# Kernel tuning notes

Measured on AMD Instinct MI355X. Metric: run time of the kernel, lower is better.

Reference implementation:

```python
import jax, jax.numpy as jnp
import numpy as np

ALPHA = 0.5    # SpikeAct surrogate width (act_fun(alpha=0.5))
DECAY = 0.2    # membrane decay
THRESH = 0.5   # firing threshold (requires_grad=False -> constant)


@jax.custom_vjp
def spike_act(x):
    # Heaviside spike with rectangular surrogate gradient
    return (x > 0).astype(x.dtype)

def _sa_fwd(x):
    return spike_act(x), x

def _sa_bwd(x, g):
    return (g * (jnp.abs(x) < ALPHA).astype(g.dtype),)

spike_act.defvjp(_sa_fwd, _sa_bwd)


@jax.custom_vjp
def ei_act(x):
    # EI sign gate with straight-through gradient
    return jnp.sign(x)

def _ei_fwd(x):
    return ei_act(x), None

def _ei_bwd(_, g):
    return (g,)

ei_act.defvjp(_ei_fwd, _ei_bwd)


def conv2d(x, w, b):
    # x: [B,C,H,W], w: [O,I,kh,kw] (OIHW), SAME padding, stride 1
    y = jax.lax.conv_general_dilated(
        x, w, window_strides=(1, 1), padding='SAME',
        dimension_numbers=('NCHW', 'OIHW', 'NCHW'))
    return y + b[None, :, None, None]


def setup_inputs() -> dict:
    key = jax.random.key(0)
    k0, k1, k2 = jax.random.split(key, 3)
    T, B, C, H, W, K = 8, 16, 128, 32, 32, 5
    fan_in = C * K * K
    x = jax.random.normal(k0, (T, B, C, H, W), jnp.float32)
    back_w = jax.random.normal(k1, (C, C, K, K), jnp.float32) / np.float32(np.sqrt(fan_in))
    back_b = jnp.zeros((C,), jnp.float32)
    ei_w = jax.random.normal(k2, (C, C, K, K), jnp.float32) / np.float32(np.sqrt(fan_in))
    ei_b = jnp.zeros((C,), jnp.float32)
    return {"x": x, "back_w": back_w, "back_b": back_b, "ei_w": ei_w, "ei_b": ei_b}


def reference(x, back_w, back_b, ei_w, ei_b):
    # x: [T,B,C,H,W] -> spikes over time [T,B,C,H,W]
    state_shape = x.shape[1:]
    mem0 = jnp.zeros(state_shape, x.dtype)
    spike0 = jnp.zeros(state_shape, x.dtype)

    def step(carry, xt):
        mem, spike = carry
        # integral: decayed mem + feedback-conv sigmoid gate * input
        mem = DECAY * mem + jax.nn.sigmoid(conv2d(spike, back_w, back_b)) * xt
        # calc_spike (if_ei=True path)
        ei_gate = ei_act(conv2d(mem, ei_w, ei_b))
        s = spike_act(mem - THRESH)
        mem = mem * (1.0 - s)
        spike = ei_gate * s
        return (mem, spike), spike

    _, spikes = jax.lax.scan(step, (mem0, spike0), x)
    return spikes
```

## Files before the change

kernel.cpp:

```cpp
#include <hip/hip_runtime.h>
#include <math.h>

#define TDIM 512
#define CCH  128
#define HW   32
#define OCT  4
#define ICT  4
#define NPH  16
#define SW   36
#define SROWS 36
#define PLANE (SROWS * SW)

template<int EPI>
__global__ __launch_bounds__(TDIM, 2) void lif_conv(
    const float* __restrict__ cin,
    const float* __restrict__ wgt,
    const float* __restrict__ bias,
    const float* __restrict__ aux0,
    const float* __restrict__ aux1,
    float* __restrict__ out0,
    float* __restrict__ out1,
    int first)
{
    const int ocg  = blockIdx.x;
    const int b    = blockIdx.y;
    const int oc0  = ocg * OCT;
    const int tid  = threadIdx.x;
    const int team = tid >> 8;
    const int lt   = tid & 255;
    const int rl   = lt >> 3;
    const int cl   = (lt & 7) * 4;

    const int steam = __builtin_amdgcn_readfirstlane(team);

    __shared__ __align__(16) float s_in[2 * ICT * PLANE];
    float* tin = s_in + team * (ICT * PLANE);

    float acc[OCT][4];
#pragma unroll
    for (int oc = 0; oc < OCT; ++oc)
#pragma unroll
        for (int j = 0; j < 4; ++j) acc[oc][j] = 0.f;

    if (!(EPI == 0 && first)) {
        const int icbase  = team * 64;
        const int sicbase = steam * 64;
        for (int i = lt; i < ICT * PLANE; i += 256) tin[i] = 0.f;
        __syncthreads();

        const int sr = lt >> 3;
        const int sg = lt & 7;

        for (int ph = 0; ph < NPH; ++ph) {
#pragma unroll
            for (int p = 0; p < ICT; ++p) {
                float4 v = *(const float4*)&cin[(((size_t)b * CCH + icbase + ph * ICT + p) * HW + sr) * HW + sg * 4];
                float* dst = &tin[p * PLANE + (sr + 2) * SW + 2 + sg * 4];
                *(float2*)dst       = make_float2(v.x, v.y);
                *(float2*)(dst + 2) = make_float2(v.z, v.w);
            }
            __syncthreads();
#pragma unroll
            for (int ici = 0; ici < ICT; ++ici) {
                float win5[5][8];
#pragma unroll
                for (int kh = 0; kh < 5; ++kh) {
                    const float* src = &tin[ici * PLANE + (rl + kh) * SW + cl];
                    float4 a = *(const float4*)src;
                    float4 c = *(const float4*)(src + 4);
                    win5[kh][0] = a.x; win5[kh][1] = a.y; win5[kh][2] = a.z; win5[kh][3] = a.w;
                    win5[kh][4] = c.x; win5[kh][5] = c.y; win5[kh][6] = c.z; win5[kh][7] = c.w;
                }
                const float* wb = wgt + ((size_t)oc0 * CCH + sicbase + ph * ICT + ici) * 25;
#pragma unroll
                for (int oc = 0; oc < OCT; ++oc) {
                    const float* wo = wb + oc * (CCH * 25);
#pragma unroll
                    for (int kh = 0; kh < 5; ++kh) {
#pragma unroll
                        for (int kw = 0; kw < 5; ++kw) {
                            float wv = wo[kh * 5 + kw];
                            acc[oc][0] += win5[kh][kw]     * wv;
                            acc[oc][1] += win5[kh][kw + 1] * wv;
                            acc[oc][2] += win5[kh][kw + 2] * wv;
                            acc[oc][3] += win5[kh][kw + 3] * wv;
                        }
                    }
                }
            }
            __syncthreads();
        }

        float* sred = s_in;
        if (team == 1) {
#pragma unroll
            for (int oc = 0; oc < OCT; ++oc)
#pragma unroll
                for (int j = 0; j < 4; ++j)
                    sred[lt * 17 + oc * 4 + j] = acc[oc][j];
        }
        __syncthreads();
        if (team == 0) {
#pragma unroll
            for (int oc = 0; oc < OCT; ++oc)
#pragma unroll
                for (int j = 0; j < 4; ++j)
                    acc[oc][j] += sred[lt * 17 + oc * 4 + j];
        }
    }

    if (team == 0) {
#pragma unroll
        for (int oc = 0; oc < OCT; ++oc) {
            const size_t pidx = (((size_t)b * CCH + oc0 + oc) * HW + rl) * HW + cl;
            const float bia = bias[oc0 + oc];
            float y[4];
#pragma unroll
            for (int j = 0; j < 4; ++j) y[j] = acc[oc][j] + bia;
            if (EPI == 0) {
                float4 xv = *(const float4*)(aux1 + pidx);
                float4 mv;
                if (first) { mv.x = mv.y = mv.z = mv.w = 0.f; }
                else       mv = *(const float4*)(aux0 + pidx);
                float4 mp;
                mp.x = 0.2f * mv.x + (1.f / (1.f + expf(-y[0]))) * xv.x;
                mp.y = 0.2f * mv.y + (1.f / (1.f + expf(-y[1]))) * xv.y;
                mp.z = 0.2f * mv.z + (1.f / (1.f + expf(-y[2]))) * xv.z;
                mp.w = 0.2f * mv.w + (1.f / (1.f + expf(-y[3]))) * xv.w;
                *(float4*)(out0 + pidx) = mp;
            } else {
                float4 m4 = *(const float4*)(aux0 + pidx);
                float g[4] = {
                    (y[0] > 0.f) ? 1.f : ((y[0] < 0.f) ? -1.f : 0.f),
                    (y[1] > 0.f) ? 1.f : ((y[1] < 0.f) ? -1.f : 0.f),
                    (y[2] > 0.f) ? 1.f : ((y[2] < 0.f) ? -1.f : 0.f),
                    (y[3] > 0.f) ? 1.f : ((y[3] < 0.f) ? -1.f : 0.f)};
                float m[4] = {m4.x, m4.y, m4.z, m4.w};
                float4 mn, sp;
                float s0 = (m[0] > 0.5f) ? 1.f : 0.f;
                float s1 = (m[1] > 0.5f) ? 1.f : 0.f;
                float s2 = (m[2] > 0.5f) ? 1.f : 0.f;
                float s3 = (m[3] > 0.5f) ? 1.f : 0.f;
                mn.x = m[0] * (1.f - s0); sp.x = g[0] * s0;
                mn.y = m[1] * (1.f - s1); sp.y = g[1] * s1;
                mn.z = m[2] * (1.f - s2); sp.z = g[2] * s2;
                mn.w = m[3] * (1.f - s3); sp.w = g[3] * s3;
                *(float4*)(out0 + pidx) = mn;
                *(float4*)(out1 + pidx) = sp;
            }
        }
    }
}

extern "C" void kernel_launch(void* const* d_in, const int* in_sizes, int n_in,
                              void* d_out, int out_size, void* d_ws, size_t ws_size,
                              hipStream_t stream) {
    const float* x      = (const float*)d_in[0];
    const float* back_w = (const float*)d_in[1];
    const float* back_b = (const float*)d_in[2];
    const float* ei_w   = (const float*)d_in[3];
    const float* ei_b   = (const float*)d_in[4];
    float* out = (float*)d_out;

    const size_t N = (size_t)16 * CCH * HW * HW;
    float* mem_cur  = (float*)d_ws;
    float* mem_post = mem_cur + N;

    dim3 grid(CCH / OCT, 16);

    for (int t = 0; t < 8; ++t) {
        const float* spike_prev = (t == 0) ? x : (out + (size_t)(t - 1) * N);
        lif_conv<0><<<grid, TDIM, 0, stream>>>(
            spike_prev, back_w, back_b,
            mem_cur, x + (size_t)t * N,
            mem_post, nullptr, (t == 0) ? 1 : 0);
        lif_conv<1><<<grid, TDIM, 0, stream>>>(
            mem_post, ei_w, ei_b,
            mem_post, nullptr,
            mem_cur, out + (size_t)t * N, 0);
    }
}
```

Baseline: 2.128 ms.

## Split each image into row halves and use four input-channel teams per block

```diff
diff --git a/kernel.cpp b/kernel.cpp
--- a/kernel.cpp
+++ b/kernel.cpp
@@ -5,14 +5,16 @@
 #define CCH  128
 #define HW   32
 #define OCT  4
-#define ICT  4
+#define ICT  2
 #define NPH  16
+#define NTEAM 4
+#define RPB  16
 #define SW   36
-#define SROWS 36
+#define SROWS 20
 #define PLANE (SROWS * SW)
 
 template<int EPI>
-__global__ __launch_bounds__(TDIM, 2) void lif_conv(
+__global__ __launch_bounds__(TDIM, 8) void lif_conv(
     const float* __restrict__ cin,
     const float* __restrict__ wgt,
     const float* __restrict__ bias,
@@ -23,17 +25,19 @@
     int first)
 {
     const int ocg  = blockIdx.x;
-    const int b    = blockIdx.y;
+    const int half = blockIdx.y;
+    const int b    = blockIdx.z;
     const int oc0  = ocg * OCT;
+    const int r0   = half * RPB;
     const int tid  = threadIdx.x;
-    const int team = tid >> 8;
-    const int lt   = tid & 255;
+    const int team = tid >> 7;
+    const int lt   = tid & 127;
     const int rl   = lt >> 3;
     const int cl   = (lt & 7) * 4;
 
     const int steam = __builtin_amdgcn_readfirstlane(team);
 
-    __shared__ __align__(16) float s_in[2 * ICT * PLANE];
+    __shared__ __align__(16) float s_in[NTEAM * ICT * PLANE];
     float* tin = s_in + team * (ICT * PLANE);
 
     float acc[OCT][4];
@@ -43,21 +47,24 @@
         for (int j = 0; j < 4; ++j) acc[oc][j] = 0.f;
 
     if (!(EPI == 0 && first)) {
-        const int icbase  = team * 64;
-        const int sicbase = steam * 64;
-        for (int i = lt; i < ICT * PLANE; i += 256) tin[i] = 0.f;
-        __syncthreads();
-
-        const int sr = lt >> 3;
-        const int sg = lt & 7;
+        const int icbase  = team * 32;
+        const int sicbase = steam * 32;
+        for (int i = tid; i < NTEAM * ICT * PLANE; i += TDIM) s_in[i] = 0.f;
+        __syncthreads();
 
         for (int ph = 0; ph < NPH; ++ph) {
-#pragma unroll
-            for (int p = 0; p < ICT; ++p) {
-                float4 v = *(const float4*)&cin[(((size_t)b * CCH + icbase + ph * ICT + p) * HW + sr) * HW + sg * 4];
-                float* dst = &tin[p * PLANE + (sr + 2) * SW + 2 + sg * 4];
-                *(float2*)dst       = make_float2(v.x, v.y);
-                *(float2*)(dst + 2) = make_float2(v.z, v.w);
+            for (int idx = lt; idx < ICT * SROWS * 8; idx += 128) {
+                int p    = idx / (SROWS * 8);
+                int rem  = idx - p * (SROWS * 8);
+                int srow = rem >> 3;
+                int sg   = rem & 7;
+                int gr   = r0 + srow - 2;
+                if (gr >= 0 && gr < HW) {
+                    float4 v = *(const float4*)&cin[(((size_t)b * CCH + icbase + ph * ICT + p) * HW + gr) * HW + sg * 4];
+                    float* dst = &tin[p * PLANE + srow * SW + 2 + sg * 4];
+                    *(float2*)dst       = make_float2(v.x, v.y);
+                    *(float2*)(dst + 2) = make_float2(v.z, v.w);
+                }
             }
             __syncthreads();
 #pragma unroll
@@ -91,28 +98,42 @@
             __syncthreads();
         }
 
-        float* sred = s_in;
-        if (team == 1) {
+        float* red = s_in;
+        if (team == 1)
+#pragma unroll
+            for (int oc = 0; oc < OCT; ++oc)
+#pragma unroll
+                for (int j = 0; j < 4; ++j) red[lt * 17 + oc * 4 + j] = acc[oc][j];
+        if (team == 2)
+#pragma unroll
+            for (int oc = 0; oc < OCT; ++oc)
+#pragma unroll
+                for (int j = 0; j < 4; ++j) red[128 * 17 + lt * 17 + oc * 4 + j] = acc[oc][j];
+        __syncthreads();
+        if (team == 0)
 #pragma unroll
             for (int oc = 0; oc < OCT; ++oc)
 #pragma unroll
                 for (int j = 0; j < 4; ++j)
-                    sred[lt * 17 + oc * 4 + j] = acc[oc][j];
-        }
-        __syncthreads();
-        if (team == 0) {
-#pragma unroll
-            for (int oc = 0; oc < OCT; ++oc)
-#pragma unroll
-                for (int j = 0; j < 4; ++j)
-                    acc[oc][j] += sred[lt * 17 + oc * 4 + j];
-        }
+                    acc[oc][j] += red[lt * 17 + oc * 4 + j] + red[128 * 17 + lt * 17 + oc * 4 + j];
+        __syncthreads();
+        if (team == 3)
+#pragma unroll
+            for (int oc = 0; oc < OCT; ++oc)
+#pragma unroll
+                for (int j = 0; j < 4; ++j) red[lt * 17 + oc * 4 + j] = acc[oc][j];
+        __syncthreads();
+        if (team == 0)
+#pragma unroll
+            for (int oc = 0; oc < OCT; ++oc)
+#pragma unroll
+                for (int j = 0; j < 4; ++j) acc[oc][j] += red[lt * 17 + oc * 4 + j];
     }
 
     if (team == 0) {
 #pragma unroll
         for (int oc = 0; oc < OCT; ++oc) {
-            const size_t pidx = (((size_t)b * CCH + oc0 + oc) * HW + rl) * HW + cl;
+            const size_t pidx = (((size_t)b * CCH + oc0 + oc) * HW + (r0 + rl)) * HW + cl;
             const float bia = bias[oc0 + oc];
             float y[4];
 #pragma unroll
@@ -166,7 +187,7 @@
     float* mem_cur  = (float*)d_ws;
     float* mem_post = mem_cur + N;
 
-    dim3 grid(CCH / OCT, 16);
+    dim3 grid(CCH / OCT, 2, 16);
 
     for (int t = 0; t < 8; ++t) {
         const float* spike_prev = (t == 0) ? x : (out + (size_t)(t - 1) * N);
```

Measured after the change: 2.369 ms. +11.3%, slower.

## Keep state in padded layout and double-buffer conv input via global_load_lds

Applied to the files above, without the earlier changes.

```diff
diff --git a/kernel.cpp b/kernel.cpp
--- a/kernel.cpp
+++ b/kernel.cpp
@@ -5,21 +5,28 @@
 #define CCH  128
 #define HW   32
 #define OCT  4
-#define ICT  4
-#define NPH  16
-#define SW   36
-#define SROWS 36
-#define PLANE (SROWS * SW)
+#define NPH  32
+#define PSW  36
+#define PPL  1296
+#define NCHK 11
+#define LDSPH 2816
+
+
+__device__ __forceinline__ void gll16(const float* g, float* l) {
+    __builtin_amdgcn_global_load_lds(
+        (const __attribute__((address_space(1))) unsigned int*)g,
+        (__attribute__((address_space(3))) unsigned int*)l, 16, 0, 0);
+}
 
 template<int EPI>
 __global__ __launch_bounds__(TDIM, 2) void lif_conv(
-    const float* __restrict__ cin,
+    const float* __restrict__ cpad,
     const float* __restrict__ wgt,
     const float* __restrict__ bias,
-    const float* __restrict__ aux0,
-    const float* __restrict__ aux1,
-    float* __restrict__ out0,
-    float* __restrict__ out1,
+    const float* __restrict__ xin,
+    float* __restrict__ pad0,
+    float* __restrict__ outn,
+    float* __restrict__ pad1,
     int first)
 {
     const int ocg  = blockIdx.x;
@@ -30,11 +37,12 @@
     const int lt   = tid & 255;
     const int rl   = lt >> 3;
     const int cl   = (lt & 7) * 4;
+    const int wv   = (tid >> 6) & 3;
+    const int lane = tid & 63;
 
     const int steam = __builtin_amdgcn_readfirstlane(team);
 
-    __shared__ __align__(16) float s_in[2 * ICT * PLANE];
-    float* tin = s_in + team * (ICT * PLANE);
+    __shared__ __align__(16) float s_in[2 * 2 * LDSPH];
 
     float acc[OCT][4];
 #pragma unroll
@@ -43,35 +51,37 @@
         for (int j = 0; j < 4; ++j) acc[oc][j] = 0.f;
 
     if (!(EPI == 0 && first)) {
-        const int icbase  = team * 64;
-        const int sicbase = steam * 64;
-        for (int i = lt; i < ICT * PLANE; i += 256) tin[i] = 0.f;
-        __syncthreads();
+        const int icb  = team * 64;
+        const int sicb = steam * 64;
+        float* lbase = s_in + steam * (2 * LDSPH);
 
-        const int sr = lt >> 3;
-        const int sg = lt & 7;
+        {
+            const float* ps = cpad + ((size_t)b * CCH + icb) * PPL;
+            for (int j = wv; j < NCHK; j += 4)
+                gll16(ps + j * 256 + lane * 4, lbase + j * 256);
+        }
 
         for (int ph = 0; ph < NPH; ++ph) {
+            __syncthreads();
+            if (ph < NPH - 1) {
+                const float* ps = cpad + ((size_t)b * CCH + icb + (ph + 1) * 2) * PPL;
+                float* ld = lbase + ((ph + 1) & 1) * LDSPH;
+                for (int j = wv; j < NCHK; j += 4)
+                    gll16(ps + j * 256 + lane * 4, ld + j * 256);
+            }
+            const float* tin = lbase + (ph & 1) * LDSPH;
 #pragma unroll
-            for (int p = 0; p < ICT; ++p) {
-                float4 v = *(const float4*)&cin[(((size_t)b * CCH + icbase + ph * ICT + p) * HW + sr) * HW + sg * 4];
-                float* dst = &tin[p * PLANE + (sr + 2) * SW + 2 + sg * 4];
-                *(float2*)dst       = make_float2(v.x, v.y);
-                *(float2*)(dst + 2) = make_float2(v.z, v.w);
-            }
-            __syncthreads();
-#pragma unroll
-            for (int ici = 0; ici < ICT; ++ici) {
+            for (int ici = 0; ici < 2; ++ici) {
                 float win5[5][8];
 #pragma unroll
                 for (int kh = 0; kh < 5; ++kh) {
-                    const float* src = &tin[ici * PLANE + (rl + kh) * SW + cl];
-                    float4 a = *(const float4*)src;
-                    float4 c = *(const float4*)(src + 4);
-                    win5[kh][0] = a.x; win5[kh][1] = a.y; win5[kh][2] = a.z; win5[kh][3] = a.w;
-                    win5[kh][4] = c.x; win5[kh][5] = c.y; win5[kh][6] = c.z; win5[kh][7] = c.w;
+                    const float* src = tin + ici * PPL + (rl + kh) * PSW + cl;
+                    float4 a  = *(const float4*)src;
+                    float4 c2 = *(const float4*)(src + 4);
+                    win5[kh][0] = a.x;  win5[kh][1] = a.y;  win5[kh][2] = a.z;  win5[kh][3] = a.w;
+                    win5[kh][4] = c2.x; win5[kh][5] = c2.y; win5[kh][6] = c2.z; win5[kh][7] = c2.w;
                 }
-                const float* wb = wgt + ((size_t)oc0 * CCH + sicbase + ph * ICT + ici) * 25;
+                const float* wb = wgt + ((size_t)oc0 * CCH + sicb + ph * 2 + ici) * 25;
 #pragma unroll
                 for (int oc = 0; oc < OCT; ++oc) {
                     const float* wo = wb + oc * (CCH * 25);
@@ -79,18 +89,18 @@
                     for (int kh = 0; kh < 5; ++kh) {
 #pragma unroll
                         for (int kw = 0; kw < 5; ++kw) {
-                            float wv = wo[kh * 5 + kw];
-                            acc[oc][0] += win5[kh][kw]     * wv;
-                            acc[oc][1] += win5[kh][kw + 1] * wv;
-                            acc[oc][2] += win5[kh][kw + 2] * wv;
-                            acc[oc][3] += win5[kh][kw + 3] * wv;
+                            float wv2 = wo[kh * 5 + kw];
+                            acc[oc][0] += win5[kh][kw]     * wv2;
+                            acc[oc][1] += win5[kh][kw + 1] * wv2;
+                            acc[oc][2] += win5[kh][kw + 2] * wv2;
+                            acc[oc][3] += win5[kh][kw + 3] * wv2;
                         }
                     }
                 }
             }
-            __syncthreads();
         }
 
+        __syncthreads();
         float* sred = s_in;
         if (team == 1) {
 #pragma unroll
@@ -112,41 +122,43 @@
     if (team == 0) {
 #pragma unroll
         for (int oc = 0; oc < OCT; ++oc) {
-            const size_t pidx = (((size_t)b * CCH + oc0 + oc) * HW + rl) * HW + cl;
+            const size_t pidxn = (((size_t)b * CCH + oc0 + oc) * HW + rl) * HW + cl;
+            const size_t pidxp = ((size_t)b * CCH + oc0 + oc) * PPL + (rl + 2) * PSW + 2 + cl;
             const float bia = bias[oc0 + oc];
             float y[4];
 #pragma unroll
             for (int j = 0; j < 4; ++j) y[j] = acc[oc][j] + bia;
             if (EPI == 0) {
-                float4 xv = *(const float4*)(aux1 + pidx);
-                float4 mv;
-                if (first) { mv.x = mv.y = mv.z = mv.w = 0.f; }
-                else       mv = *(const float4*)(aux0 + pidx);
-                float4 mp;
-                mp.x = 0.2f * mv.x + (1.f / (1.f + expf(-y[0]))) * xv.x;
-                mp.y = 0.2f * mv.y + (1.f / (1.f + expf(-y[1]))) * xv.y;
-                mp.z = 0.2f * mv.z + (1.f / (1.f + expf(-y[2]))) * xv.z;
-                mp.w = 0.2f * mv.w + (1.f / (1.f + expf(-y[3]))) * xv.w;
-                *(float4*)(out0 + pidx) = mp;
+                float4 xv = *(const float4*)(xin + pidxn);
+                float xr[4] = {xv.x, xv.y, xv.z, xv.w};
+                float mo[4] = {0.f, 0.f, 0.f, 0.f};
+                if (!first) {
+                    float2 a = *(const float2*)(pad0 + pidxp);
+                    float2 c = *(const float2*)(pad0 + pidxp + 2);
+                    mo[0] = a.x; mo[1] = a.y; mo[2] = c.x; mo[3] = c.y;
+                }
+                float mp[4];
+#pragma unroll
+                for (int j = 0; j < 4; ++j) {
+                    float mv = (mo[j] > 0.5f) ? 0.f : mo[j];
+                    mp[j] = 0.2f * mv + (1.f / (1.f + expf(-y[j]))) * xr[j];
+                }
+                *(float2*)(pad0 + pidxp)     = make_float2(mp[0], mp[1]);
+                *(float2*)(pad0 + pidxp + 2) = make_float2(mp[2], mp[3]);
             } else {
-                float4 m4 = *(const float4*)(aux0 + pidx);
-                float g[4] = {
-                    (y[0] > 0.f) ? 1.f : ((y[0] < 0.f) ? -1.f : 0.f),
-                    (y[1] > 0.f) ? 1.f : ((y[1] < 0.f) ? -1.f : 0.f),
-                    (y[2] > 0.f) ? 1.f : ((y[2] < 0.f) ? -1.f : 0.f),
-                    (y[3] > 0.f) ? 1.f : ((y[3] < 0.f) ? -1.f : 0.f)};
-                float m[4] = {m4.x, m4.y, m4.z, m4.w};
-                float4 mn, sp;
-                float s0 = (m[0] > 0.5f) ? 1.f : 0.f;
-                float s1 = (m[1] > 0.5f) ? 1.f : 0.f;
-                float s2 = (m[2] > 0.5f) ? 1.f : 0.f;
-                float s3 = (m[3] > 0.5f) ? 1.f : 0.f;
-                mn.x = m[0] * (1.f - s0); sp.x = g[0] * s0;
-                mn.y = m[1] * (1.f - s1); sp.y = g[1] * s1;
-                mn.z = m[2] * (1.f - s2); sp.z = g[2] * s2;
-                mn.w = m[3] * (1.f - s3); sp.w = g[3] * s3;
-                *(float4*)(out0 + pidx) = mn;
-                *(float4*)(out1 + pidx) = sp;
+                float2 a = *(const float2*)(pad0 + pidxp);
+                float2 c = *(const float2*)(pad0 + pidxp + 2);
+                float m[4] = {a.x, a.y, c.x, c.y};
+                float sp[4];
+#pragma unroll
+                for (int j = 0; j < 4; ++j) {
+                    float g = (y[j] > 0.f) ? 1.f : ((y[j] < 0.f) ? -1.f : 0.f);
+                    float s = (m[j] > 0.5f) ? 1.f : 0.f;
+                    sp[j] = g * s;
+                }
+                *(float4*)(outn + pidxn) = make_float4(sp[0], sp[1], sp[2], sp[3]);
+                *(float2*)(pad1 + pidxp)     = make_float2(sp[0], sp[1]);
+                *(float2*)(pad1 + pidxp + 2) = make_float2(sp[2], sp[3]);
             }
         }
     }
@@ -162,21 +174,23 @@
     const float* ei_b   = (const float*)d_in[4];
     float* out = (float*)d_out;
 
-    const size_t N = (size_t)16 * CCH * HW * HW;
-    float* mem_cur  = (float*)d_ws;
-    float* mem_post = mem_cur + N;
+    const size_t N     = (size_t)16 * CCH * HW * HW;
+    const size_t PADSZ = (size_t)16 * CCH * PPL;
+    float* pad0 = (float*)d_ws;
+    float* pad1 = pad0 + PADSZ;
+
+    hipMemsetAsync(d_ws, 0, 2 * PADSZ * sizeof(float), stream);
 
     dim3 grid(CCH / OCT, 16);
 
     for (int t = 0; t < 8; ++t) {
-        const float* spike_prev = (t == 0) ? x : (out + (size_t)(t - 1) * N);
         lif_conv<0><<<grid, TDIM, 0, stream>>>(
-            spike_prev, back_w, back_b,
-            mem_cur, x + (size_t)t * N,
-            mem_post, nullptr, (t == 0) ? 1 : 0);
+            pad1, back_w, back_b,
+            x + (size_t)t * N,
+            pad0, nullptr, nullptr, (t == 0) ? 1 : 0);
         lif_conv<1><<<grid, TDIM, 0, stream>>>(
-            mem_post, ei_w, ei_b,
-            mem_post, nullptr,
-            mem_cur, out + (size_t)t * N, 0);
+            pad0, ei_w, ei_b,
+            nullptr,
+            pad0, out + (size_t)t * N, pad1, 0);
     }
 }
```

After: 2.272 ms. 1.07x slower.
